# Optimization experiments

Hardware: AMD Instinct MI355X
Metric: run time of the kernel (lower is better)

## Reference

```python
import jax, jax.numpy as jnp
import numpy as np
from jax import lax

N = 10000
E = 320000
FLAT = 32 * 10 * 32  # conv channels * pooled 20x64 -> 10x32


def setup_inputs() -> dict:
    key = jax.random.key(0)
    ks = jax.random.split(key, 16)
    s = 0.05
    return {
        "features": jax.random.normal(ks[0], (N, 20, 64), jnp.float32),
        "src": jax.random.randint(ks[1], (E,), 0, N, jnp.int32),
        "dst": jax.random.randint(ks[2], (E,), 0, N, jnp.int32),
        # CNN params
        "conv_w": jax.random.normal(ks[3], (32, 1, 3, 3), jnp.float32) * s,
        "conv_b": jnp.zeros((32,), jnp.float32),
        "w1": jax.random.normal(ks[4], (FLAT, 32), jnp.float32) * s,
        "b1": jnp.zeros((32,), jnp.float32),
        "w2": jax.random.normal(ks[5], (32, 32), jnp.float32) * s,
        "b2": jnp.zeros((32,), jnp.float32),
        # SAGEConv1 (32 -> 64)
        "s1_self": jax.random.normal(ks[6], (32, 64), jnp.float32) * s,
        "s1_neigh": jax.random.normal(ks[7], (32, 64), jnp.float32) * s,
        "s1_b": jnp.zeros((64,), jnp.float32),
        # SAGEConv2 (64 -> 10)
        "s2_self": jax.random.normal(ks[8], (64, 10), jnp.float32) * s,
        "s2_neigh": jax.random.normal(ks[9], (64, 10), jnp.float32) * s,
        "s2_b": jnp.zeros((10,), jnp.float32),
    }


def _cnn(x, conv_w, conv_b, w1, b1, w2, b2):
    # x: [N, 1, 20, 64]
    x = lax.conv_general_dilated(x, conv_w, (1, 1), "SAME",
                                 dimension_numbers=("NCHW", "OIHW", "NCHW"))
    x = jax.nn.relu(x + conv_b[None, :, None, None])
    x = lax.reduce_window(x, -jnp.inf, lax.max, (1, 1, 2, 2), (1, 1, 2, 2), "VALID")
    x = x.reshape(x.shape[0], -1)  # [N, FLAT], NCHW flatten matches torch
    x = jax.nn.relu(x @ w1 + b1)
    x = jax.nn.relu(x @ w2 + b2)
    return x


def _sage_mean(x, src, dst, w_self, w_neigh, b):
    # DGL SAGEConv 'mean': mean over in-neighbors (messages src->dst)
    agg = jax.ops.segment_sum(x[src], dst, num_segments=N)
    deg = jax.ops.segment_sum(jnp.ones((src.shape[0],), x.dtype), dst, num_segments=N)
    agg = agg / jnp.maximum(deg, 1.0)[:, None]
    return x @ w_self + agg @ w_neigh + b


def reference(features, src, dst, conv_w, conv_b, w1, b1, w2, b2,
              s1_self, s1_neigh, s1_b, s2_self, s2_neigh, s2_b):
    h = _cnn(features[:, None, :, :], conv_w, conv_b, w1, b1, w2, b2)  # [N, 32]
    h = jax.nn.relu(_sage_mean(h, src, dst, s1_self, s1_neigh, s1_b))  # [N, 64]
    out = _sage_mean(h, src, dst, s2_self, s2_neigh, s2_b)             # [N, 10]
    return out
```

## Files before the change

### kernel.cpp

```cpp
#include <hip/hip_runtime.h>


typedef __attribute__((ext_vector_type(8)))  short bf16x8;
typedef __attribute__((ext_vector_type(4)))  float f32x4;
typedef __attribute__((ext_vector_type(16))) float f32x16;

__device__ __forceinline__ unsigned short f2bf(float v) {
    union { float f; unsigned int u; } x; x.f = v;
    unsigned int r = x.u + 0x7FFFu + ((x.u >> 16) & 1u);
    return (unsigned short)(r >> 16);
}
__device__ __forceinline__ float bf2f(unsigned short b) {
    union { float f; unsigned int u; } x; x.u = ((unsigned int)b) << 16;
    return x.f;
}
__device__ __forceinline__ unsigned cvtpk(float a, float b) {
    unsigned r;
    asm("v_cvt_pk_bf16_f32 %0, %1, %2" : "=v"(r) : "v"(a), "v"(b));
    return r;
}
__device__ __forceinline__ float lo2f(unsigned p) { union { unsigned u; float f; } x; x.u = p << 16; return x.f; }
__device__ __forceinline__ float hi2f(unsigned p) { union { unsigned u; float f; } x; x.u = p & 0xffff0000u; return x.f; }
__device__ __forceinline__ void split_pair(float a, float b, unsigned& hp, unsigned& lp) {
    hp = cvtpk(a, b);
    lp = cvtpk(a - lo2f(hp), b - hi2f(hp));
}

__global__ __launch_bounds__(256) void zero_ws(float* __restrict__ ws, int count) {
    int i = blockIdx.x * 256 + threadIdx.x;
    if (i < count) ws[i] = 0.0f;
}

__global__ __launch_bounds__(256) void w1_prep_v3(
    const float* __restrict__ w1, unsigned char* __restrict__ w1f)
{
    int gu = blockIdx.x * 256 + threadIdx.x;
    const int quarter = gu >> 11;
    const int u = gu & 2047;
    const int ph = quarter >> 2, qq = quarter & 3;
    const int ks   = u >> 8;
    const int jh   = (u >> 7) & 1;
    const int part = (u >> 6) & 1;
    const int lane = u & 63;
    const int j    = jh * 16 + (lane & 15);
    const int c    = ks * 4 + (lane >> 4);
    const int k0   = c * 320 + ph * 32 + qq * 8;
    unsigned short v[8];
#pragma unroll
    for (int i = 0; i < 8; ++i) {
        float x = w1[(size_t)(k0 + i) * 32 + j];
        unsigned short h = f2bf(x);
        v[i] = part ? f2bf(x - bf2f(h)) : h;
    }
    *(uint4*)(w1f + (size_t)quarter * 32768 + (size_t)u * 16) = *(const uint4*)v;
}

__global__ __launch_bounds__(256, 3) void cnn_fused_v9(
    const float* __restrict__ feat,
    const float* __restrict__ conv_w, const float* __restrict__ conv_b,
    const unsigned char* __restrict__ w1f,
    float* __restrict__ h_fc1)
{
    __shared__ __align__(16) unsigned char convA[18432];
    __shared__ __align__(16) unsigned char fc1A[32768];

    const int t = threadIdx.x;
    const int wv = t >> 6;
    const int lane = t & 63;
    const int base = blockIdx.x * 16;
    const int qq = blockIdx.y;

    const int nn  = lane >> 4;
    const int pwl = lane & 7;
    const int aa  = (lane >> 3) & 1;
    const float* featn = feat + (size_t)(base + wv * 4 + nn) * 1280;

    const int pw = qq * 8 + pwl;
    const int c0 = 2 * pw - 1;
    const bool cv0 = (c0 >= 0);
    const bool cv3 = (c0 + 3 < 64);

    const int cch = lane & 31;
    const int ckg = lane >> 5;
    const int rowr = lane & 31;
    unsigned rsw = (unsigned)(rowr << 4); rsw ^= ((rsw >> 7) & 3u) << 4;

    bf16x8 cbh, cbl;
    {
        union { unsigned short u[8]; bf16x8 v; } H, L;
#pragma unroll
        for (int i = 0; i < 8; ++i) {
            int k = ckg * 8 + i;
            float x = (k < 9) ? conv_w[cch * 9 + k] : 0.0f;
            unsigned short h = f2bf(x);
            H.u[i] = h; L.u[i] = f2bf(x - bf2f(h));
        }
        cbh = H.v; cbl = L.v;
    }
    const float cbias = conv_b[cch];

    const int nfr = lane & 15;

    f32x4 acc0 = {0.f, 0.f, 0.f, 0.f};
    f32x4 acc1 = {0.f, 0.f, 0.f, 0.f};

    float f0[4], f1[4], f2[4];
    auto load_row = [&](int r, float* o) {
        bool rv = (r >= 0) && (r < 20);
        const float* rp = featn + (rv ? r : 0) * 64;
        float v0 = rp[cv0 ? c0 : 0];
        float v1 = rp[c0 + 1];
        float v2 = rp[c0 + 2];
        float v3 = rp[cv3 ? (c0 + 3) : 0];
        o[0] = (rv && cv0) ? v0 : 0.f;
        o[1] = rv ? v1 : 0.f;
        o[2] = rv ? v2 : 0.f;
        o[3] = (rv && cv3) ? v3 : 0.f;
    };

    load_row(aa - 1, f0);
    load_row(aa,     f1);
    load_row(aa + 1, f2);

#pragma unroll 1
    for (int ph = 0; ph < 10; ++ph) {
        const int quarter = ph * 4 + qq;
        unsigned char* fbuf = fc1A + ((ph & 1) << 14);

        const unsigned char* wq = w1f + (size_t)quarter * 32768;
        bf16x8 bF[2][2][2];
#pragma unroll
        for (int si = 0; si < 2; ++si) {
            const int ks = wv + si * 4;
#pragma unroll
            for (int jh = 0; jh < 2; ++jh)
#pragma unroll
                for (int part = 0; part < 2; ++part)
                    bF[si][jh][part] = *(const bf16x8*)(
                        wq + (size_t)((((ks * 2 + jh) * 2 + part)) << 10) + lane * 16);
        }

        {
            unsigned P[3][2], Q[3][2];
            split_pair(f0[0], f0[1], P[0][0], Q[0][0]);
            split_pair(f0[2], f0[3], P[0][1], Q[0][1]);
            split_pair(f1[0], f1[1], P[1][0], Q[1][0]);
            split_pair(f1[2], f1[3], P[1][1], Q[1][1]);
            split_pair(f2[0], f2[1], P[2][0], Q[2][0]);
            split_pair(f2[2], f2[3], P[2][1], Q[2][1]);

            const int r0 = pwl * 4 + aa * 2, r1 = r0 + 1;
            unsigned b0 = (unsigned)(r0 << 4); b0 ^= ((b0 >> 7) & 3u) << 4;
            unsigned b1 = (unsigned)(r1 << 4); b1 ^= ((b1 >> 7) & 3u) << 4;
            unsigned char* abw = convA + ((wv * 4 + nn) << 10);
            uint4 H0 = make_uint4(P[0][0],
                                  __builtin_amdgcn_perm(P[1][0], P[0][1], 0x05040100u),
                                  __builtin_amdgcn_perm(P[1][1], P[1][0], 0x05040302u),
                                  P[2][0]);
            uint4 H1 = make_uint4(__builtin_amdgcn_perm(P[0][1], P[0][0], 0x05040302u),
                                  __builtin_amdgcn_perm(P[1][0], P[0][1], 0x07060302u),
                                  P[1][1],
                                  __builtin_amdgcn_perm(P[2][1], P[2][0], 0x05040302u));
            uint4 L0 = make_uint4(Q[0][0],
                                  __builtin_amdgcn_perm(Q[1][0], Q[0][1], 0x05040100u),
                                  __builtin_amdgcn_perm(Q[1][1], Q[1][0], 0x05040302u),
                                  Q[2][0]);
            uint4 L1 = make_uint4(__builtin_amdgcn_perm(Q[0][1], Q[0][0], 0x05040302u),
                                  __builtin_amdgcn_perm(Q[1][0], Q[0][1], 0x07060302u),
                                  Q[1][1],
                                  __builtin_amdgcn_perm(Q[2][1], Q[2][0], 0x05040302u));
            *(uint4*)(abw + b0)       = H0;
            *(uint4*)(abw + b1)       = H1;
            *(uint4*)(abw + 512 + b0) = L0;
            *(uint4*)(abw + 512 + b1) = L1;
            unsigned wr0 = __builtin_amdgcn_perm(Q[2][1], P[2][1], 0x05040100u);
            unsigned wr1 = __builtin_amdgcn_perm(Q[2][1], P[2][1], 0x07060302u);
            *(uint2*)(convA + 16384 + (((wv * 4 + nn) * 32 + r0) << 2)) = make_uint2(wr0, wr1);
        }

        if (ph < 9) {
#pragma unroll
            for (int j = 0; j < 4; ++j) f0[j] = f2[j];
            load_row(2 * ph + 2 + aa, f1);
            load_row(2 * ph + 3 + aa, f2);
        }

#pragma unroll
        for (int nn2 = 0; nn2 < 4; ++nn2) {
            bf16x8 a_h, a_l;
            if (ckg == 0) {
                const unsigned char* ab = convA + ((wv * 4 + nn2) << 10);
                a_h = *(const bf16x8*)(ab + rsw);
                a_l = *(const bf16x8*)(ab + 512 + rsw);
            } else {
                unsigned cw = *(const unsigned*)(convA + 16384 + (((wv * 4 + nn2) * 32 + rowr) << 2));
                a_h = (bf16x8){(short)(cw & 0xffffu), 0, 0, 0, 0, 0, 0, 0};
                a_l = (bf16x8){(short)(cw >> 16),     0, 0, 0, 0, 0, 0, 0};
            }
            f32x16 ca = {};
            ca = __builtin_amdgcn_mfma_f32_32x32x16_bf16(a_l, cbh, ca, 0, 0, 0);
            ca = __builtin_amdgcn_mfma_f32_32x32x16_bf16(a_h, cbl, ca, 0, 0, 0);
            ca = __builtin_amdgcn_mfma_f32_32x32x16_bf16(a_h, cbh, ca, 0, 0, 0);

            float pv0 = fmaxf(fmaxf(fmaxf(ca[0],  ca[1]),  fmaxf(ca[2],  ca[3]))  + cbias, 0.f);
            float pv1 = fmaxf(fmaxf(fmaxf(ca[4],  ca[5]),  fmaxf(ca[6],  ca[7]))  + cbias, 0.f);
            float pv2 = fmaxf(fmaxf(fmaxf(ca[8],  ca[9]),  fmaxf(ca[10], ca[11])) + cbias, 0.f);
            float pv3 = fmaxf(fmaxf(fmaxf(ca[12], ca[13]), fmaxf(ca[14], ca[15])) + cbias, 0.f);

            unsigned ha, la, hb, lb;
            split_pair(pv0, pv1, ha, la);
            split_pair(pv2, pv3, hb, lb);
            unsigned pha = (unsigned)__shfl_xor((int)ha, 32);
            unsigned phb = (unsigned)__shfl_xor((int)hb, 32);
            unsigned pla = (unsigned)__shfl_xor((int)la, 32);
            unsigned plb = (unsigned)__shfl_xor((int)lb, 32);
            bool hih = (lane < 32);
            unsigned q0v = hih ? pha : la;
            unsigned q1v = hih ? ha  : pla;
            unsigned q2v = hih ? phb : lb;
            unsigned q3v = hih ? hb  : plb;
            unsigned w0  = __builtin_amdgcn_perm(q0v, q1v, 0x05040100u);
            unsigned w1v = __builtin_amdgcn_perm(q0v, q1v, 0x07060302u);
            unsigned w2v = __builtin_amdgcn_perm(q2v, q3v, 0x05040100u);
            unsigned w3v = __builtin_amdgcn_perm(q2v, q3v, 0x07060302u);
            const int nloc = wv * 4 + nn2;
            const int pS = hih ? 0 : 1;
            const int ksW = cch >> 2, kgW = cch & 3;
            unsigned byteW = (unsigned)((((pS * 8 + ksW) * 64) + kgW * 16 + nloc) << 4);
            byteW ^= ((byteW >> 8) & 7u) << 4;
            *(uint4*)(fbuf + byteW) = make_uint4(w0, w1v, w2v, w3v);
        }

        __syncthreads();

#pragma unroll
        for (int si = 0; si < 2; ++si) {
            const int ks = wv + si * 4;
            unsigned bH = (unsigned)(((0 * 8 + ks) << 10) + lane * 16); bH ^= ((bH >> 8) & 7u) << 4;
            unsigned bL = (unsigned)(((1 * 8 + ks) << 10) + lane * 16); bL ^= ((bL >> 8) & 7u) << 4;
            bf16x8 fa_h = *(const bf16x8*)(fbuf + bH);
            bf16x8 fa_l = *(const bf16x8*)(fbuf + bL);
            acc0 = __builtin_amdgcn_mfma_f32_16x16x32_bf16(fa_l, bF[si][0][0], acc0, 0, 0, 0);
            acc0 = __builtin_amdgcn_mfma_f32_16x16x32_bf16(fa_h, bF[si][0][1], acc0, 0, 0, 0);
            acc0 = __builtin_amdgcn_mfma_f32_16x16x32_bf16(fa_h, bF[si][0][0], acc0, 0, 0, 0);
            acc1 = __builtin_amdgcn_mfma_f32_16x16x32_bf16(fa_l, bF[si][1][0], acc1, 0, 0, 0);
            acc1 = __builtin_amdgcn_mfma_f32_16x16x32_bf16(fa_h, bF[si][1][1], acc1, 0, 0, 0);
            acc1 = __builtin_amdgcn_mfma_f32_16x16x32_bf16(fa_h, bF[si][1][0], acc1, 0, 0, 0);
        }
    }

    __syncthreads();
    float* red = (float*)convA;
#pragma unroll
    for (int r = 0; r < 4; ++r) {
        int node = (lane >> 4) * 4 + r;
        red[wv * 512 + node * 32 + nfr]      = acc0[r];
        red[wv * 512 + node * 32 + 16 + nfr] = acc1[r];
    }
    __syncthreads();
    {
        const int en = t >> 4, jp = t & 15;
        const int j0 = 2 * jp;
        float s0 = 0.f, s1 = 0.f;
#pragma unroll
        for (int wi = 0; wi < 4; ++wi) {
            s0 += red[wi * 512 + en * 32 + j0];
            s1 += red[wi * 512 + en * 32 + j0 + 1];
        }
        atomicAdd(&h_fc1[(size_t)(base + en) * 32 + j0],     s0);
        atomicAdd(&h_fc1[(size_t)(base + en) * 32 + j0 + 1], s1);
    }
}

__global__ __launch_bounds__(256) void fc1_finish(
    const float* __restrict__ h_fc1, const float* __restrict__ b1,
    const float* __restrict__ w2, const float* __restrict__ b2,
    float* __restrict__ h_out, int N)
{
    __shared__ float hr[8][32];
    const int t = threadIdx.x;
    const int nb = t >> 5, j = t & 31;
    const int n = blockIdx.x * 8 + nb;
    if (n < N) hr[nb][j] = fmaxf(h_fc1[(size_t)n * 32 + j] + b1[j], 0.f);
    __syncthreads();
    if (n >= N) return;
    float o = b2[j];
#pragma unroll
    for (int k = 0; k < 32; ++k) o = fmaf(hr[nb][k], w2[k * 32 + j], o);
    h_out[(size_t)n * 32 + j] = fmaxf(o, 0.f);
}

__global__ __launch_bounds__(256) void count_deg(
    const int* __restrict__ dst, int* __restrict__ cnt, int E)
{
    int e = blockIdx.x * 256 + threadIdx.x;
    if (e < E) atomicAdd(&cnt[dst[e]], 1);
}

__global__ __launch_bounds__(256) void scan_local(
    const int* __restrict__ cnt, int* __restrict__ excl, int* __restrict__ bsum, int N)
{
    __shared__ int s[256];
    int t = threadIdx.x, b = blockIdx.x, i = b * 256 + t;
    int v = (i < N) ? cnt[i] : 0;
    s[t] = v;
    __syncthreads();
#pragma unroll
    for (int off = 1; off < 256; off <<= 1) {
        int x = (t >= off) ? s[t - off] : 0;
        __syncthreads();
        s[t] += x;
        __syncthreads();
    }
    int incl = s[t];
    if (i < N) excl[i] = incl - v;
    if (t == 255) bsum[b] = incl;
}

__global__ __launch_bounds__(64) void scan_bsum(
    const int* __restrict__ bsum, int* __restrict__ bsumx, int* __restrict__ row_ptr,
    int nb, int N)
{
    int t = threadIdx.x;
    int v = (t < nb) ? bsum[t] : 0;
    int incl = v;
#pragma unroll
    for (int off = 1; off < 64; off <<= 1) {
        int x = __shfl_up(incl, off);
        if (t >= off) incl += x;
    }
    if (t < nb) bsumx[t] = incl - v;
    if (t == 63) row_ptr[N] = incl;
}

__global__ __launch_bounds__(256) void scan_add(
    const int* __restrict__ excl, const int* __restrict__ bsumx,
    int* __restrict__ row_ptr, int* __restrict__ cursor, int N)
{
    int i = blockIdx.x * 256 + threadIdx.x;
    if (i < N) {
        int rp = excl[i] + bsumx[i >> 8];
        row_ptr[i] = rp;
        cursor[i]  = rp;
    }
}

__global__ __launch_bounds__(256) void fill_csr(
    const int* __restrict__ src, const int* __restrict__ dst,
    int* __restrict__ cursor, int* __restrict__ csr, int E)
{
    int e = blockIdx.x * 256 + threadIdx.x;
    if (e >= E) return;
    int idx = atomicAdd(&cursor[dst[e]], 1);
    csr[idx] = src[e];
}

__global__ __launch_bounds__(256) void sage1_fused(
    const float* __restrict__ h, const int* __restrict__ rp, const int* __restrict__ csr,
    const float* __restrict__ s1_self, const float* __restrict__ s1_neigh,
    const float* __restrict__ s1_b, const float* __restrict__ s2_neigh,
    float* __restrict__ h1, float* __restrict__ z16, int N)
{
    __shared__ float aggs[4][32];
    __shared__ float hl[4][64];
    const int t = threadIdx.x;
    const int nb = t >> 6, k = t & 63;
    const int n = blockIdx.x * 4 + nb;
    const int j = k & 31, half = k >> 5;

    int p0 = 0, p1 = 0;
    if (n < N) { p0 = rp[n]; p1 = rp[n + 1]; }
    float a = 0.f;
    for (int p = p0 + half; p < p1; p += 2)
        a += h[(size_t)csr[p] * 32 + j];
    a += __shfl_down(a, 32);
    if (half == 0) aggs[nb][j] = a;
    __syncthreads();

    float o = 0.f;
    if (n < N) {
        const int nu = __builtin_amdgcn_readfirstlane(n);
        float inv = 1.0f / fmaxf((float)(p1 - p0), 1.0f);
        o = s1_b[k];
#pragma unroll
        for (int jj = 0; jj < 32; ++jj) {
            o = fmaf(h[(size_t)nu * 32 + jj], s1_self[jj * 64 + k], o);
            o = fmaf(aggs[nb][jj] * inv, s1_neigh[jj * 64 + k], o);
        }
        o = fmaxf(o, 0.f);
        h1[(size_t)n * 64 + k] = o;
    }
    hl[nb][k] = o;
    __syncthreads();

    if (n < N && k < 16) {
        float z = 0.f;
        if (k < 10) {
#pragma unroll
            for (int jj = 0; jj < 64; ++jj) z = fmaf(hl[nb][jj], s2_neigh[jj * 10 + k], z);
        }
        z16[(size_t)n * 16 + k] = z;
    }
}

__global__ __launch_bounds__(256) void sage2_final_g(
    const float* __restrict__ h1, const float* __restrict__ z16,
    const int* __restrict__ rp, const int* __restrict__ csr,
    const float* __restrict__ s2_self, const float* __restrict__ s2_b,
    float* __restrict__ out, int N)
{
    int tid = blockIdx.x * 256 + threadIdx.x;
    int nn = tid >> 4, k = tid & 15;
    if (nn >= N || k >= 10) return;
    int p0 = rp[nn], p1 = rp[nn + 1];
    float a0 = 0.f, a1 = 0.f;
    int p = p0;
    for (; p + 2 <= p1; p += 2) {
        int s0 = csr[p], s1 = csr[p + 1];
        a0 += z16[(size_t)s0 * 16 + k];
        a1 += z16[(size_t)s1 * 16 + k];
    }
    if (p < p1) a0 += z16[(size_t)csr[p] * 16 + k];
    float inv = 1.0f / fmaxf((float)(p1 - p0), 1.0f);
    float o = s2_b[k] + (a0 + a1) * inv;
#pragma unroll
    for (int j = 0; j < 64; ++j) o = fmaf(h1[nn * 64 + j], s2_self[j * 10 + k], o);
    out[nn * 10 + k] = o;
}

extern "C" void kernel_launch(void* const* d_in, const int* in_sizes, int n_in,
                              void* d_out, int out_size, void* d_ws, size_t ws_size,
                              hipStream_t stream)
{
    const float* feat     = (const float*)d_in[0];
    const int*   src      = (const int*)d_in[1];
    const int*   dst      = (const int*)d_in[2];
    const float* conv_w   = (const float*)d_in[3];
    const float* conv_b   = (const float*)d_in[4];
    const float* w1       = (const float*)d_in[5];
    const float* b1       = (const float*)d_in[6];
    const float* w2       = (const float*)d_in[7];
    const float* b2       = (const float*)d_in[8];
    const float* s1_self  = (const float*)d_in[9];
    const float* s1_neigh = (const float*)d_in[10];
    const float* s1_b     = (const float*)d_in[11];
    const float* s2_self  = (const float*)d_in[12];
    const float* s2_neigh = (const float*)d_in[13];
    const float* s2_b     = (const float*)d_in[14];
    float* out = (float*)d_out;

    const int N = in_sizes[0] / 1280;
    const int E = in_sizes[1];
    const int NB_SCAN = (N + 255) / 256;

    char* wsb = (char*)d_ws;
    int*   row_cnt = (int*)wsb;                      wsb += (size_t)N * 4;
    float* h_fc1   = (float*)wsb;                    wsb += (size_t)N * 32 * 4;
    int*   excl    = (int*)wsb;                      wsb += (size_t)N * 4;
    int*   bsum    = (int*)wsb;                      wsb += 64 * 4;
    int*   bsumx   = (int*)wsb;                      wsb += 64 * 4;
    int*   row_ptr = (int*)wsb;                      wsb += (size_t)(N + 4) * 4;
    int*   cursor  = (int*)wsb;                      wsb += (size_t)N * 4;
    int*   csr     = (int*)wsb;                      wsb += (size_t)E * 4;
    float* h_cnn   = (float*)wsb;                    wsb += (size_t)N * 32 * 4;
    float* h1      = (float*)wsb;                    wsb += (size_t)N * 64 * 4;
    float* z16     = (float*)wsb;                    wsb += (size_t)N * 16 * 4;
    unsigned char* w1f = (unsigned char*)wsb;

    zero_ws<<<(33 * N + 255) / 256, 256, 0, stream>>>((float*)row_cnt, 33 * N);

    count_deg<<<(E + 255) / 256, 256, 0, stream>>>(dst, row_cnt, E);
    scan_local<<<NB_SCAN, 256, 0, stream>>>(row_cnt, excl, bsum, N);
    scan_bsum<<<1, 64, 0, stream>>>(bsum, bsumx, row_ptr, NB_SCAN, N);
    scan_add<<<NB_SCAN, 256, 0, stream>>>(excl, bsumx, row_ptr, cursor, N);
    fill_csr<<<(E + 255) / 256, 256, 0, stream>>>(src, dst, cursor, csr, E);

    w1_prep_v3<<<320, 256, 0, stream>>>(w1, w1f);
    dim3 cg(N / 16, 4);
    cnn_fused_v9<<<cg, 256, 0, stream>>>(feat, conv_w, conv_b, w1f, h_fc1);
    fc1_finish<<<(N + 7) / 8, 256, 0, stream>>>(h_fc1, b1, w2, b2, h_cnn, N);

    sage1_fused<<<(N + 3) / 4, 256, 0, stream>>>(
        h_cnn, row_ptr, csr, s1_self, s1_neigh, s1_b, s2_neigh, h1, z16, N);

    sage2_final_g<<<(int)(((size_t)N * 16 + 255) / 256), 256, 0, stream>>>(
        h1, z16, row_ptr, csr, s2_self, s2_b, out, N);
}
```

Before: 209.1 us.

## Prefetch feature rows a phase ahead and merge CSR scan into one kernel

The CNN kernel now loads input feature rows one phase early into extra registers, fully unrolls the phase loop, and reads the two middle columns with a float2 load. This is meant to hide global-load latency behind MFMA work. The three-kernel prefix scan is replaced by a single-block scan where each thread handles 40 counts, removing two launches. Full unrolling and the extra row buffers raise register pressure under launch_bounds(256,3), and the single-block scan hardcodes 256*40 elements, so it only covers N up to 10240.

```diff
diff --git a/kernel.cpp b/kernel.cpp
--- a/kernel.cpp
+++ b/kernel.cpp
@@ -55,7 +55,7 @@
     *(uint4*)(w1f + (size_t)quarter * 32768 + (size_t)u * 16) = *(const uint4*)v;
 }
 
-__global__ __launch_bounds__(256, 3) void cnn_fused_v9(
+__global__ __launch_bounds__(256, 3) void cnn_fused_v10(
     const float* __restrict__ feat,
     const float* __restrict__ conv_w, const float* __restrict__ conv_b,
     const unsigned char* __restrict__ w1f,
@@ -103,26 +103,28 @@
 
     f32x4 acc0 = {0.f, 0.f, 0.f, 0.f};
     f32x4 acc1 = {0.f, 0.f, 0.f, 0.f};
-
-    float f0[4], f1[4], f2[4];
+    const f32x16 czero = {};
+
+    float f0[4], f1[4], f2[4], g1[4], g2[4];
     auto load_row = [&](int r, float* o) {
         bool rv = (r >= 0) && (r < 20);
         const float* rp = featn + (rv ? r : 0) * 64;
+        float2 m = *(const float2*)(rp + c0 + 1);
         float v0 = rp[cv0 ? c0 : 0];
-        float v1 = rp[c0 + 1];
-        float v2 = rp[c0 + 2];
         float v3 = rp[cv3 ? (c0 + 3) : 0];
         o[0] = (rv && cv0) ? v0 : 0.f;
-        o[1] = rv ? v1 : 0.f;
-        o[2] = rv ? v2 : 0.f;
+        o[1] = rv ? m.x : 0.f;
+        o[2] = rv ? m.y : 0.f;
         o[3] = (rv && cv3) ? v3 : 0.f;
     };
 
     load_row(aa - 1, f0);
     load_row(aa,     f1);
     load_row(aa + 1, f2);
-
-#pragma unroll 1
+    load_row(aa + 2, g1);
+    load_row(aa + 3, g2);
+
+#pragma unroll
     for (int ph = 0; ph < 10; ++ph) {
         const int quarter = ph * 4 + qq;
         unsigned char* fbuf = fc1A + ((ph & 1) << 14);
@@ -180,9 +182,11 @@
 
         if (ph < 9) {
 #pragma unroll
-            for (int j = 0; j < 4; ++j) f0[j] = f2[j];
-            load_row(2 * ph + 2 + aa, f1);
-            load_row(2 * ph + 3 + aa, f2);
+            for (int j = 0; j < 4; ++j) { f0[j] = f2[j]; f1[j] = g1[j]; f2[j] = g2[j]; }
+        }
+        if (ph < 8) {
+            load_row(2 * ph + 4 + aa, g1);
+            load_row(2 * ph + 5 + aa, g2);
         }
 
 #pragma unroll
@@ -197,8 +201,8 @@
                 a_h = (bf16x8){(short)(cw & 0xffffu), 0, 0, 0, 0, 0, 0, 0};
                 a_l = (bf16x8){(short)(cw >> 16),     0, 0, 0, 0, 0, 0, 0};
             }
-            f32x16 ca = {};
-            ca = __builtin_amdgcn_mfma_f32_32x32x16_bf16(a_l, cbh, ca, 0, 0, 0);
+            f32x16 ca;
+            ca = __builtin_amdgcn_mfma_f32_32x32x16_bf16(a_l, cbh, czero, 0, 0, 0);
             ca = __builtin_amdgcn_mfma_f32_32x32x16_bf16(a_h, cbl, ca, 0, 0, 0);
             ca = __builtin_amdgcn_mfma_f32_32x32x16_bf16(a_h, cbh, ca, 0, 0, 0);
 
@@ -297,52 +301,41 @@
     if (e < E) atomicAdd(&cnt[dst[e]], 1);
 }
 
-__global__ __launch_bounds__(256) void scan_local(
-    const int* __restrict__ cnt, int* __restrict__ excl, int* __restrict__ bsum, int N)
-{
-    __shared__ int s[256];
-    int t = threadIdx.x, b = blockIdx.x, i = b * 256 + t;
-    int v = (i < N) ? cnt[i] : 0;
-    s[t] = v;
+__global__ __launch_bounds__(256) void scan_all(
+    const int* __restrict__ cnt, int* __restrict__ row_ptr, int* __restrict__ cursor, int N)
+{
+    __shared__ int ps[256];
+    const int t = threadIdx.x;
+    const int base = t * 40;
+    int vals[40];
+    int run = 0;
+#pragma unroll
+    for (int i = 0; i < 40; ++i) {
+        int idx = base + i;
+        int v = (idx < N) ? cnt[idx] : 0;
+        vals[i] = run;
+        run += v;
+    }
+    ps[t] = run;
     __syncthreads();
 #pragma unroll
     for (int off = 1; off < 256; off <<= 1) {
-        int x = (t >= off) ? s[t - off] : 0;
+        int x = (t >= off) ? ps[t - off] : 0;
         __syncthreads();
-        s[t] += x;
+        ps[t] += x;
         __syncthreads();
     }
-    int incl = s[t];
-    if (i < N) excl[i] = incl - v;
-    if (t == 255) bsum[b] = incl;
-}
-
-__global__ __launch_bounds__(64) void scan_bsum(
-    const int* __restrict__ bsum, int* __restrict__ bsumx, int* __restrict__ row_ptr,
-    int nb, int N)
-{
-    int t = threadIdx.x;
-    int v = (t < nb) ? bsum[t] : 0;
-    int incl = v;
-#pragma unroll
-    for (int off = 1; off < 64; off <<= 1) {
-        int x = __shfl_up(incl, off);
-        if (t >= off) incl += x;
-    }
-    if (t < nb) bsumx[t] = incl - v;
-    if (t == 63) row_ptr[N] = incl;
-}
-
-__global__ __launch_bounds__(256) void scan_add(
-    const int* __restrict__ excl, const int* __restrict__ bsumx,
-    int* __restrict__ row_ptr, int* __restrict__ cursor, int N)
-{
-    int i = blockIdx.x * 256 + threadIdx.x;
-    if (i < N) {
-        int rp = excl[i] + bsumx[i >> 8];
-        row_ptr[i] = rp;
-        cursor[i]  = rp;
-    }
+    int excl = ps[t] - run;
+#pragma unroll
+    for (int i = 0; i < 40; ++i) {
+        int idx = base + i;
+        if (idx < N) {
+            int rp = excl + vals[i];
+            row_ptr[idx] = rp;
+            cursor[idx]  = rp;
+        }
+    }
+    if (t == 255) row_ptr[N] = ps[255];
 }
 
 __global__ __launch_bounds__(256) void fill_csr(
@@ -451,14 +444,10 @@
 
     const int N = in_sizes[0] / 1280;
     const int E = in_sizes[1];
-    const int NB_SCAN = (N + 255) / 256;
 
     char* wsb = (char*)d_ws;
     int*   row_cnt = (int*)wsb;                      wsb += (size_t)N * 4;
     float* h_fc1   = (float*)wsb;                    wsb += (size_t)N * 32 * 4;
-    int*   excl    = (int*)wsb;                      wsb += (size_t)N * 4;
-    int*   bsum    = (int*)wsb;                      wsb += 64 * 4;
-    int*   bsumx   = (int*)wsb;                      wsb += 64 * 4;
     int*   row_ptr = (int*)wsb;                      wsb += (size_t)(N + 4) * 4;
     int*   cursor  = (int*)wsb;                      wsb += (size_t)N * 4;
     int*   csr     = (int*)wsb;                      wsb += (size_t)E * 4;
@@ -470,14 +459,12 @@
     zero_ws<<<(33 * N + 255) / 256, 256, 0, stream>>>((float*)row_cnt, 33 * N);
 
     count_deg<<<(E + 255) / 256, 256, 0, stream>>>(dst, row_cnt, E);
-    scan_local<<<NB_SCAN, 256, 0, stream>>>(row_cnt, excl, bsum, N);
-    scan_bsum<<<1, 64, 0, stream>>>(bsum, bsumx, row_ptr, NB_SCAN, N);
-    scan_add<<<NB_SCAN, 256, 0, stream>>>(excl, bsumx, row_ptr, cursor, N);
+    scan_all<<<1, 256, 0, stream>>>(row_cnt, row_ptr, cursor, N);
     fill_csr<<<(E + 255) / 256, 256, 0, stream>>>(src, dst, cursor, csr, E);
 
     w1_prep_v3<<<320, 256, 0, stream>>>(w1, w1f);
     dim3 cg(N / 16, 4);
-    cnn_fused_v9<<<cg, 256, 0, stream>>>(feat, conv_w, conv_b, w1f, h_fc1);
+    cnn_fused_v10<<<cg, 256, 0, stream>>>(feat, conv_w, conv_b, w1f, h_fc1);
     fc1_finish<<<(N + 7) / 8, 256, 0, stream>>>(h_fc1, b1, w2, b2, h_cnn, N);
 
     sage1_fused<<<(N + 3) / 4, 256, 0, stream>>>(
```

Result: no change. 211.1 us (+0.9%).
